# Kernel optimization log

Measured on AMD Instinct MI355X. Metric: run time of the kernel, lower is better.

## Reference

```python
import jax, jax.numpy as jnp
import numpy as np

N_HEADS = 16
D_MODEL = 1024
D_K = D_MODEL // N_HEADS
NEG_INF = -1e9


def setup_inputs() -> dict:
    key = jax.random.key(0)
    ks = jax.random.split(key, 7)
    B, S, D = 4, 2048, D_MODEL
    scale = 1.0 / np.sqrt(D)
    return {
        "query": jax.random.normal(ks[0], (B, S, D), dtype=jnp.float32),
        "key": jax.random.normal(ks[1], (B, S, D), dtype=jnp.float32),
        "value": jax.random.normal(ks[2], (B, S, D), dtype=jnp.float32),
        "Wq": jax.random.normal(ks[3], (D, D), dtype=jnp.float32) * scale,
        "Wk": jax.random.normal(ks[4], (D, D), dtype=jnp.float32) * scale,
        "Wv": jax.random.normal(ks[5], (D, D), dtype=jnp.float32) * scale,
        "Wo": jax.random.normal(ks[6], (D, D), dtype=jnp.float32) * scale,
    }


def _split_heads(x):
    # (B, S, D) -> (B, H, S, d_k)
    B, S, _ = x.shape
    return x.reshape(B, S, N_HEADS, D_K).transpose(0, 2, 1, 3)


def reference(query, key, value, Wq, Wk, Wv, Wo):
    B, S, D = query.shape
    # nn.Linear(d, d, bias=False): y = x @ W.T ; here W is stored as [out, in]
    Q = _split_heads(query @ Wq.T)
    K = _split_heads(key @ Wk.T)
    V = _split_heads(value @ Wv.T)
    scores = jnp.einsum("bhqd,bhkd->bhqk", Q, K) / jnp.sqrt(jnp.float32(D_K))
    # causal mask: 0 on/below diagonal, -1e9 above
    causal = jnp.where(
        jnp.tril(jnp.ones((S, S), dtype=bool)), 0.0, NEG_INF
    ).astype(scores.dtype)
    scores = scores + causal[None, None, :, :]
    attn = jax.nn.softmax(scores, axis=-1)
    heads = jnp.einsum("bhqk,bhkd->bhqd", attn, V)
    concat = heads.transpose(0, 2, 1, 3).reshape(B, S, D)
    out = concat @ Wo.T
    return out  # dropout p=0.0 -> identity
```

## Files before the change

### kernel.cpp

```cpp
#include <hip/hip_runtime.h>
#include <hip/hip_bf16.h>

typedef short short8 __attribute__((ext_vector_type(8)));
typedef short short4v __attribute__((ext_vector_type(4)));
typedef float floatx4 __attribute__((ext_vector_type(4)));

constexpr int BATCH = 4;
constexpr int SEQ = 2048;
constexpr int DMODEL = 1024;
constexpr int NHEADS = 16;
constexpr int DKH = 64;
constexpr int MROWS = BATCH * SEQ;
constexpr size_t NE = (size_t)MROWS * DMODEL;
constexpr size_t WE = (size_t)DMODEL * DMODEL;
constexpr float SC = 0.18033688011112042f;

__device__ __forceinline__ short f2bf(float f) {
    unsigned u = __float_as_uint(f);
    u += 0x7fffu + ((u >> 16) & 1u);
    return (short)(u >> 16);
}

__device__ __forceinline__ short2 pk2(float a, float b) {
    __hip_bfloat162 h = __float22bfloat162_rn(float2{a, b});
    short2 r;
    __builtin_memcpy(&r, &h, 4);
    return r;
}

__device__ __forceinline__ void ld16(const void* g, void* l) {
    __builtin_amdgcn_global_load_lds(
        (const __attribute__((address_space(1))) unsigned int*)g,
        (__attribute__((address_space(3))) unsigned int*)l, 16, 0, 0);
}

__device__ __forceinline__ void sync_vm4() {
    asm volatile("s_waitcnt vmcnt(4)" ::: "memory");
    __builtin_amdgcn_sched_barrier(0);
    __builtin_amdgcn_s_barrier();
    __builtin_amdgcn_sched_barrier(0);
}
__device__ __forceinline__ void sync_vm0() {
    asm volatile("s_waitcnt vmcnt(0)" ::: "memory");
    __builtin_amdgcn_sched_barrier(0);
    __builtin_amdgcn_s_barrier();
    __builtin_amdgcn_sched_barrier(0);
}

__global__ __launch_bounds__(256) void f32_to_bf16(const float* __restrict__ s,
                                                   short* __restrict__ d, int n4) {
    int i = blockIdx.x * blockDim.x + threadIdx.x;
    const int stride = gridDim.x * blockDim.x;
    for (; i < n4; i += stride) {
        float4 f = ((const float4*)s)[i];
        short4v v;
        v[0] = f2bf(f.x); v[1] = f2bf(f.y); v[2] = f2bf(f.z); v[3] = f2bf(f.w);
        ((short4v*)d)[i] = v;
    }
}

__global__ __launch_bounds__(256) void cvt2(const float* __restrict__ s0,
                                            const float* __restrict__ s1,
                                            short* __restrict__ d0,
                                            short* __restrict__ d1, int n4) {
    const float* s = blockIdx.y ? s1 : s0;
    short* d = blockIdx.y ? d1 : d0;
    int i = blockIdx.x * blockDim.x + threadIdx.x;
    const int stride = gridDim.x * blockDim.x;
    for (; i < n4; i += stride) {
        float4 f = ((const float4*)s)[i];
        short4v v;
        v[0] = f2bf(f.x); v[1] = f2bf(f.y); v[2] = f2bf(f.z); v[3] = f2bf(f.w);
        ((short4v*)d)[i] = v;
    }
}

__global__ __launch_bounds__(256) void wcvt3(const float* __restrict__ a,
                                             const float* __restrict__ b,
                                             const float* __restrict__ c,
                                             short* __restrict__ dst, int n4) {
    const float* s = (blockIdx.y == 0) ? a : (blockIdx.y == 1) ? b : c;
    const float m = (blockIdx.y == 0) ? SC : 1.0f;
    short* d = dst + (size_t)blockIdx.y * (size_t)n4 * 4;
    int i = blockIdx.x * blockDim.x + threadIdx.x;
    const int stride = gridDim.x * blockDim.x;
    for (; i < n4; i += stride) {
        float4 f = ((const float4*)s)[i];
        short4v v;
        v[0] = f2bf(f.x * m); v[1] = f2bf(f.y * m);
        v[2] = f2bf(f.z * m); v[3] = f2bf(f.w * m);
        ((short4v*)d)[i] = v;
    }
}

template <int MH, int KS, bool RB>
__device__ __forceinline__ void do_phase(const short* Ab, const short* Bb,
                                         floatx4 (&acc)[8][4], short8 (&bfr)[4],
                                         int wmw, int wnw, int lane16, int quad,
                                         int fsw) {
    if (RB) {
#pragma unroll
        for (int ni = 0; ni < 4; ++ni) {
            const int row = wnw + ni * 16 + lane16;
            bfr[ni] = *(const short8*)&Bb[KS * (256 * 32) + row * 32 +
                                          ((quad ^ fsw) * 8)];
        }
    }
    short8 af[4];
#pragma unroll
    for (int i = 0; i < 4; ++i) {
        const int row = wmw + MH * 64 + i * 16 + lane16;
        af[i] = *(const short8*)&Ab[KS * (256 * 32) + row * 32 +
                                    ((quad ^ fsw) * 8)];
    }
    __builtin_amdgcn_s_setprio(1);
#pragma unroll
    for (int i = 0; i < 4; ++i)
#pragma unroll
        for (int ni = 0; ni < 4; ++ni)
            acc[MH * 4 + i][ni] = __builtin_amdgcn_mfma_f32_16x16x32_bf16(
                af[i], bfr[ni], acc[MH * 4 + i][ni], 0, 0, 0);
    __builtin_amdgcn_s_setprio(0);
}

template <int OUT_MODE>
__device__ __forceinline__ void gemm_body(const short* A, const short* B,
                                          void* Yp) {
    __shared__ __align__(16) short Asw[2][2][256 * 32];
    __shared__ __align__(16) short Bsw[2][2][256 * 32];

    const int tid = threadIdx.x;
    const int w = tid >> 6, l = tid & 63;
    const int lane16 = l & 15, quad = l >> 4;
    const int wmw = (w >> 2) * 128, wnw = (w & 3) * 64;
    const int m0 = blockIdx.x * 256, n0 = blockIdx.y * 256;
    const int fsw = (lane16 >> 1) & 3;

    const int rr = tid >> 2;
    const int cc = (tid & 3) ^ ((rr >> 1) & 3);
    const int ldsA0 = (w * 64) * 8, ldsA1 = (512 + w * 64) * 8;

    auto stA = [&](int k0, int bufi, int ks) {
        const short* g = A + (size_t)m0 * DMODEL + k0 + ks * 32 + cc * 8;
        ld16(g + (size_t)rr * DMODEL, &Asw[bufi][ks][ldsA0]);
        ld16(g + (size_t)(rr + 128) * DMODEL, &Asw[bufi][ks][ldsA1]);
    };
    auto stB = [&](int k0, int bufi, int ks) {
        const short* g = B + (size_t)n0 * DMODEL + k0 + ks * 32 + cc * 8;
        ld16(g + (size_t)rr * DMODEL, &Bsw[bufi][ks][ldsA0]);
        ld16(g + (size_t)(rr + 128) * DMODEL, &Bsw[bufi][ks][ldsA1]);
    };

    floatx4 acc[8][4];
#pragma unroll
    for (int i = 0; i < 8; ++i)
#pragma unroll
        for (int j = 0; j < 4; ++j) acc[i][j] = {0.f, 0.f, 0.f, 0.f};

    constexpr int NT = DMODEL / 64;
    stA(0, 0, 0); stB(0, 0, 0); stA(0, 0, 1); stB(0, 0, 1);
    sync_vm4();

    short8 bfr[4];
    for (int t = 0; t < NT; ++t) {
        const int cur = t & 1, nxt = cur ^ 1;
        const short* Ab = &Asw[cur][0][0];
        const short* Bb = &Bsw[cur][0][0];
        const int k1 = (t + 1) * 64;
        const bool more = (t + 1 < NT);

        if (more) stA(k1, nxt, 0);
        do_phase<0, 0, true>(Ab, Bb, acc, bfr, wmw, wnw, lane16, quad, fsw);
        if (more) stB(k1, nxt, 0);
        do_phase<1, 0, false>(Ab, Bb, acc, bfr, wmw, wnw, lane16, quad, fsw);
        if (more) sync_vm4(); else sync_vm0();
        if (more) stA(k1, nxt, 1);
        do_phase<0, 1, true>(Ab, Bb, acc, bfr, wmw, wnw, lane16, quad, fsw);
        if (more) stB(k1, nxt, 1);
        do_phase<1, 1, false>(Ab, Bb, acc, bfr, wmw, wnw, lane16, quad, fsw);
        if (more) sync_vm4();
    }

    const int gmb = m0 + wmw, gnb = n0 + wnw;
    if (OUT_MODE == 0) {
        short* Y = (short*)Yp;
#pragma unroll
        for (int mi = 0; mi < 8; ++mi)
#pragma unroll
            for (int ni = 0; ni < 4; ++ni) {
                const int gm = gmb + mi * 16 + quad * 4;
                const int gn = gnb + ni * 16 + lane16;
#pragma unroll
                for (int r = 0; r < 4; ++r)
                    Y[(size_t)(gm + r) * DMODEL + gn] = f2bf(acc[mi][ni][r]);
            }
    } else if (OUT_MODE == 1) {
        short* Y = (short*)Yp;
#pragma unroll
        for (int mi = 0; mi < 8; ++mi)
#pragma unroll
            for (int ni = 0; ni < 4; ++ni) {
                const int gm = gmb + mi * 16 + quad * 4;
                const int gn = gnb + ni * 16 + lane16;
                const int bb = gm >> 11, ss = gm & (SEQ - 1);
                const int hh = gn >> 6, dd = gn & 63;
                const size_t base = ((size_t)(bb * NHEADS + hh) * DKH + dd) * SEQ + ss;
                short4v vv;
#pragma unroll
                for (int r = 0; r < 4; ++r) vv[r] = f2bf(acc[mi][ni][r]);
                *(short4v*)(Y + base) = vv;
            }
    } else {
        float* Y = (float*)Yp;
#pragma unroll
        for (int mi = 0; mi < 8; ++mi)
#pragma unroll
            for (int ni = 0; ni < 4; ++ni) {
                const int gm = gmb + mi * 16 + quad * 4;
                const int gn = gnb + ni * 16 + lane16;
#pragma unroll
                for (int r = 0; r < 4; ++r)
                    Y[(size_t)(gm + r) * DMODEL + gn] = acc[mi][ni][r];
            }
    }
}

template <int OUT_MODE>
__global__ __launch_bounds__(512, 2) void gemm_nt(const short* __restrict__ A,
                                                  const short* __restrict__ B,
                                                  void* __restrict__ Yp) {
    gemm_body<OUT_MODE>(A, B, Yp);
}

__global__ __launch_bounds__(512, 2) void gemm_qk(const short* __restrict__ Aq,
                                                  const short* __restrict__ Ak,
                                                  const short* __restrict__ Wqk,
                                                  short* __restrict__ Yq,
                                                  short* __restrict__ Yk) {
    const int z = blockIdx.z;
    gemm_body<0>(z ? Ak : Aq, Wqk + (size_t)z * WE, z ? Yk : Yq);
}

__global__ __launch_bounds__(256, 4) void attn_fwd(const short* __restrict__ Qb,
                                                   const short* __restrict__ Kb,
                                                   const short* __restrict__ Vt,
                                                   short* __restrict__ Oc) {
    __shared__ __align__(16) short Kl[2][64 * 64];
    __shared__ __align__(16) short Vl[2][64 * 64];
    __shared__ __align__(16) short Plds[4][16][64];

    const int bh = blockIdx.x;
    const int qt = (int)(gridDim.y - 1) - blockIdx.y;
    const int b = bh >> 4, h = bh & 15;
    const int tid = threadIdx.x;
    const int w = tid >> 6, l = tid & 63;
    const int lane16 = l & 15, quad = l >> 4;

    const short* Qrow =
        Qb + ((size_t)b * SEQ + qt * 64 + w * 16 + lane16) * DMODEL + h * DKH;
    const short8 qf0 = *(const short8*)(Qrow + quad * 8);
    const short8 qf1 = *(const short8*)(Qrow + 32 + quad * 8);

    const int r0 = tid >> 3, c0 = tid & 7;
    const int sc0 = c0 ^ (r0 & 7);
    const short* Kg = Kb + (size_t)b * SEQ * DMODEL + h * DKH;
    const short* Vg = Vt + (size_t)bh * DKH * SEQ;

    short8 kra, krb, vra, vrb;
    kra = *(const short8*)(Kg + (size_t)r0 * DMODEL + c0 * 8);
    krb = *(const short8*)(Kg + (size_t)(r0 + 32) * DMODEL + c0 * 8);
    vra = *(const short8*)(Vg + (size_t)r0 * SEQ + c0 * 8);
    vrb = *(const short8*)(Vg + (size_t)(r0 + 32) * SEQ + c0 * 8);
    *(short8*)&Kl[0][r0 * 64 + sc0 * 8] = kra;
    *(short8*)&Kl[0][(r0 + 32) * 64 + sc0 * 8] = krb;
    *(short8*)&Vl[0][r0 * 64 + sc0 * 8] = vra;
    *(short8*)&Vl[0][(r0 + 32) * 64 + sc0 * 8] = vrb;
    if (qt > 0) {
        kra = *(const short8*)(Kg + (size_t)(64 + r0) * DMODEL + c0 * 8);
        krb = *(const short8*)(Kg + (size_t)(64 + r0 + 32) * DMODEL + c0 * 8);
        vra = *(const short8*)(Vg + (size_t)r0 * SEQ + 64 + c0 * 8);
        vrb = *(const short8*)(Vg + (size_t)(r0 + 32) * SEQ + 64 + c0 * 8);
    }

    floatx4 oacc[4];
#pragma unroll
    for (int ni = 0; ni < 4; ++ni) oacc[ni] = {0.f, 0.f, 0.f, 0.f};
    float Lp = 0.f;
    const int swz = lane16 & 7;
    const int psw = lane16 & 7;

    for (int kt = 0; kt <= qt; ++kt) {
        const int cur = kt & 1;
        __syncthreads();
        if (kt < qt) {
            const int nb = cur ^ 1;
            *(short8*)&Kl[nb][r0 * 64 + sc0 * 8] = kra;
            *(short8*)&Kl[nb][(r0 + 32) * 64 + sc0 * 8] = krb;
            *(short8*)&Vl[nb][r0 * 64 + sc0 * 8] = vra;
            *(short8*)&Vl[nb][(r0 + 32) * 64 + sc0 * 8] = vrb;
            if (kt + 1 < qt) {
                const int kn = (kt + 2) * 64;
                kra = *(const short8*)(Kg + (size_t)(kn + r0) * DMODEL + c0 * 8);
                krb = *(const short8*)(Kg + (size_t)(kn + r0 + 32) * DMODEL + c0 * 8);
                vra = *(const short8*)(Vg + (size_t)r0 * SEQ + kn + c0 * 8);
                vrb = *(const short8*)(Vg + (size_t)(r0 + 32) * SEQ + kn + c0 * 8);
            }
        }

        float p[4][4];
#pragma unroll
        for (int nt = 0; nt < 4; ++nt) {
            const short* kr = &Kl[cur][(nt * 16 + lane16) * 64];
            floatx4 st = {0.f, 0.f, 0.f, 0.f};
            st = __builtin_amdgcn_mfma_f32_16x16x32_bf16(
                *(const short8*)(kr + (quad ^ swz) * 8), qf0, st, 0, 0, 0);
            st = __builtin_amdgcn_mfma_f32_16x16x32_bf16(
                *(const short8*)(kr + ((4 + quad) ^ swz) * 8), qf1, st, 0, 0, 0);
#pragma unroll
            for (int r = 0; r < 4; ++r) p[nt][r] = st[r];
        }

#pragma unroll
        for (int nt = 0; nt < 4; ++nt)
#pragma unroll
            for (int r = 0; r < 4; ++r) p[nt][r] = __builtin_amdgcn_exp2f(p[nt][r]);

        if (kt == qt) {
            const int qloc = w * 16 + lane16;
#pragma unroll
            for (int nt = 0; nt < 4; ++nt)
#pragma unroll
                for (int r = 0; r < 4; ++r)
                    if (nt * 16 + quad * 4 + r > qloc) p[nt][r] = 0.f;
        }

        float rs01 = 0.f, rs23 = 0.f;
#pragma unroll
        for (int nt = 0; nt < 4; ++nt)
#pragma unroll
            for (int r = 0; r < 4; ++r) {
                if (nt < 2) rs01 += p[nt][r]; else rs23 += p[nt][r];
            }
        Lp += rs01 + rs23;

#pragma unroll
        for (int nt = 0; nt < 4; ++nt) {
            const short2 lo = pk2(p[nt][0], p[nt][1]);
            const short2 hi = pk2(p[nt][2], p[nt][3]);
            short4v pk;
            pk[0] = lo.x; pk[1] = lo.y; pk[2] = hi.x; pk[3] = hi.y;
            const int pch = (nt * 2 + (quad >> 1)) ^ psw;
            *(short4v*)&Plds[w][lane16][pch * 8 + (quad & 1) * 4] = pk;
        }
        const short8 pf0 = *(const short8*)&Plds[w][lane16][(quad ^ psw) * 8];
        const short8 pf1 = *(const short8*)&Plds[w][lane16][((4 + quad) ^ psw) * 8];

#pragma unroll
        for (int ni = 0; ni < 4; ++ni) {
            const short* vr = &Vl[cur][(ni * 16 + lane16) * 64];
            oacc[ni] = __builtin_amdgcn_mfma_f32_16x16x32_bf16(
                pf0, *(const short8*)(vr + (quad ^ swz) * 8), oacc[ni], 0, 0, 0);
            oacc[ni] = __builtin_amdgcn_mfma_f32_16x16x32_bf16(
                pf1, *(const short8*)(vr + ((4 + quad) ^ swz) * 8), oacc[ni], 0, 0, 0);
        }
    }

    float L = Lp + __shfl_xor(Lp, 16);
    L += __shfl_xor(L, 32);
    float linv[4];
#pragma unroll
    for (int r = 0; r < 4; ++r) linv[r] = 1.f / __shfl(L, quad * 4 + r);
#pragma unroll
    for (int r = 0; r < 4; ++r) {
        const int qg = qt * 64 + w * 16 + quad * 4 + r;
#pragma unroll
        for (int ni = 0; ni < 4; ++ni)
            Oc[((size_t)b * SEQ + qg) * DMODEL + h * DKH + ni * 16 + lane16] =
                f2bf(oacc[ni][r] * linv[r]);
    }
}

extern "C" void kernel_launch(void* const* d_in, const int* in_sizes, int n_in,
                              void* d_out, int out_size, void* d_ws, size_t ws_size,
                              hipStream_t stream) {
    const float* q = (const float*)d_in[0];
    const float* k = (const float*)d_in[1];
    const float* v = (const float*)d_in[2];
    const float* Wq = (const float*)d_in[3];
    const float* Wk = (const float*)d_in[4];
    const float* Wv = (const float*)d_in[5];
    const float* Wo = (const float*)d_in[6];

    short* Qb = (short*)d_ws;
    short* Kb = Qb + NE;
    short* Vt = Kb + NE;
    short* Cc = Vt + NE;
    short* Wqb = (short*)d_out;
    short* Wkb = Wqb + WE;
    short* Wvb = Wqb + 2 * WE;
    short* Kbf = Wqb + 3 * WE;
    short* Wob = Vt;

    dim3 gg(MROWS / 256, DMODEL / 256);
    dim3 gqk(MROWS / 256, DMODEL / 256, 2);
    dim3 ga(BATCH * NHEADS, SEQ / 64);
    const int actN4 = (int)(NE / 4), wN4 = (int)(WE / 4);

    wcvt3<<<dim3(256, 3), 256, 0, stream>>>(Wq, Wk, Wv, (short*)d_out, wN4);
    cvt2<<<dim3(1024, 2), 256, 0, stream>>>(q, k, Cc, Kbf, actN4);
    gemm_qk<<<gqk, 512, 0, stream>>>(Cc, Kbf, Wqb, Qb, Kb);
    f32_to_bf16<<<2048, 256, 0, stream>>>(v, Cc, actN4);
    gemm_nt<1><<<gg, 512, 0, stream>>>(Cc, Wvb, Vt);
    attn_fwd<<<ga, 256, 0, stream>>>(Qb, Kb, Vt, Cc);
    f32_to_bf16<<<512, 256, 0, stream>>>(Wo, Wob, wN4);
    gemm_nt<2><<<gg, 512, 0, stream>>>(Cc, Wob, d_out);
}
```

Measured before the change: 328.5 us.

## Halve GEMM N-tile to 128 so the grid covers more CUs

```diff
diff --git a/kernel.cpp b/kernel.cpp
--- a/kernel.cpp
+++ b/kernel.cpp
@@ -34,8 +34,8 @@
         (__attribute__((address_space(3))) unsigned int*)l, 16, 0, 0);
 }
 
-__device__ __forceinline__ void sync_vm4() {
-    asm volatile("s_waitcnt vmcnt(4)" ::: "memory");
+__device__ __forceinline__ void sync_vm3() {
+    asm volatile("s_waitcnt vmcnt(3)" ::: "memory");
     __builtin_amdgcn_sched_barrier(0);
     __builtin_amdgcn_s_barrier();
     __builtin_amdgcn_sched_barrier(0);
@@ -93,33 +93,26 @@
     }
 }
 
-template <int MH, int KS, bool RB>
+template <int KS>
 __device__ __forceinline__ void do_phase(const short* Ab, const short* Bb,
-                                         floatx4 (&acc)[8][4], short8 (&bfr)[4],
-                                         int wmw, int wnw, int lane16, int quad,
-                                         int fsw) {
-    if (RB) {
-#pragma unroll
-        for (int ni = 0; ni < 4; ++ni) {
-            const int row = wnw + ni * 16 + lane16;
-            bfr[ni] = *(const short8*)&Bb[KS * (256 * 32) + row * 32 +
-                                          ((quad ^ fsw) * 8)];
-        }
-    }
-    short8 af[4];
-#pragma unroll
-    for (int i = 0; i < 4; ++i) {
-        const int row = wmw + MH * 64 + i * 16 + lane16;
-        af[i] = *(const short8*)&Ab[KS * (256 * 32) + row * 32 +
+                                         floatx4 (&acc)[4][4], int wm, int wn,
+                                         int lane16, int quad, int fsw) {
+    short8 af[4], bf[4];
+#pragma unroll
+    for (int i = 0; i < 4; ++i)
+        af[i] = *(const short8*)&Ab[KS * (256 * 32) + (wm + i * 16 + lane16) * 32 +
                                     ((quad ^ fsw) * 8)];
-    }
+#pragma unroll
+    for (int j = 0; j < 4; ++j)
+        bf[j] = *(const short8*)&Bb[KS * (128 * 32) + (wn + j * 16 + lane16) * 32 +
+                                    ((quad ^ fsw) * 8)];
     __builtin_amdgcn_s_setprio(1);
 #pragma unroll
     for (int i = 0; i < 4; ++i)
 #pragma unroll
-        for (int ni = 0; ni < 4; ++ni)
-            acc[MH * 4 + i][ni] = __builtin_amdgcn_mfma_f32_16x16x32_bf16(
-                af[i], bfr[ni], acc[MH * 4 + i][ni], 0, 0, 0);
+        for (int j = 0; j < 4; ++j)
+            acc[i][j] = __builtin_amdgcn_mfma_f32_16x16x32_bf16(af[i], bf[j],
+                                                                acc[i][j], 0, 0, 0);
     __builtin_amdgcn_s_setprio(0);
 }
 
@@ -127,41 +120,41 @@
 __device__ __forceinline__ void gemm_body(const short* A, const short* B,
                                           void* Yp) {
     __shared__ __align__(16) short Asw[2][2][256 * 32];
-    __shared__ __align__(16) short Bsw[2][2][256 * 32];
+    __shared__ __align__(16) short Bsw[2][2][128 * 32];
 
     const int tid = threadIdx.x;
     const int w = tid >> 6, l = tid & 63;
     const int lane16 = l & 15, quad = l >> 4;
-    const int wmw = (w >> 2) * 128, wnw = (w & 3) * 64;
-    const int m0 = blockIdx.x * 256, n0 = blockIdx.y * 256;
+    const int wm = (w >> 1) * 64, wn = (w & 1) * 64;
+    const int m0 = blockIdx.x * 256, n0 = blockIdx.y * 128;
     const int fsw = (lane16 >> 1) & 3;
 
     const int rr = tid >> 2;
     const int cc = (tid & 3) ^ ((rr >> 1) & 3);
-    const int ldsA0 = (w * 64) * 8, ldsA1 = (512 + w * 64) * 8;
+    const int ldsW0 = (w * 16) * 32;
+    const int ldsW1 = (128 + w * 16) * 32;
 
     auto stA = [&](int k0, int bufi, int ks) {
-        const short* g = A + (size_t)m0 * DMODEL + k0 + ks * 32 + cc * 8;
-        ld16(g + (size_t)rr * DMODEL, &Asw[bufi][ks][ldsA0]);
-        ld16(g + (size_t)(rr + 128) * DMODEL, &Asw[bufi][ks][ldsA1]);
+        const short* g = A + (size_t)(m0 + rr) * DMODEL + k0 + ks * 32 + cc * 8;
+        ld16(g, &Asw[bufi][ks][ldsW0]);
+        ld16(g + (size_t)128 * DMODEL, &Asw[bufi][ks][ldsW1]);
     };
     auto stB = [&](int k0, int bufi, int ks) {
-        const short* g = B + (size_t)n0 * DMODEL + k0 + ks * 32 + cc * 8;
-        ld16(g + (size_t)rr * DMODEL, &Bsw[bufi][ks][ldsA0]);
-        ld16(g + (size_t)(rr + 128) * DMODEL, &Bsw[bufi][ks][ldsA1]);
+        const short* g = B + (size_t)(n0 + rr) * DMODEL + k0 + ks * 32 + cc * 8;
+        ld16(g, &Bsw[bufi][ks][ldsW0]);
     };
 
-    floatx4 acc[8][4];
-#pragma unroll
-    for (int i = 0; i < 8; ++i)
+    floatx4 acc[4][4];
+#pragma unroll
+    for (int i = 0; i < 4; ++i)
 #pragma unroll
         for (int j = 0; j < 4; ++j) acc[i][j] = {0.f, 0.f, 0.f, 0.f};
 
     constexpr int NT = DMODEL / 64;
-    stA(0, 0, 0); stB(0, 0, 0); stA(0, 0, 1); stB(0, 0, 1);
-    sync_vm4();
-
-    short8 bfr[4];
+    stA(0, 0, 0); stB(0, 0, 0);
+    stA(0, 0, 1); stB(0, 0, 1);
+    sync_vm3();
+
     for (int t = 0; t < NT; ++t) {
         const int cur = t & 1, nxt = cur ^ 1;
         const short* Ab = &Asw[cur][0][0];
@@ -169,23 +162,19 @@
         const int k1 = (t + 1) * 64;
         const bool more = (t + 1 < NT);
 
-        if (more) stA(k1, nxt, 0);
-        do_phase<0, 0, true>(Ab, Bb, acc, bfr, wmw, wnw, lane16, quad, fsw);
-        if (more) stB(k1, nxt, 0);
-        do_phase<1, 0, false>(Ab, Bb, acc, bfr, wmw, wnw, lane16, quad, fsw);
-        if (more) sync_vm4(); else sync_vm0();
-        if (more) stA(k1, nxt, 1);
-        do_phase<0, 1, true>(Ab, Bb, acc, bfr, wmw, wnw, lane16, quad, fsw);
-        if (more) stB(k1, nxt, 1);
-        do_phase<1, 1, false>(Ab, Bb, acc, bfr, wmw, wnw, lane16, quad, fsw);
-        if (more) sync_vm4();
-    }
-
-    const int gmb = m0 + wmw, gnb = n0 + wnw;
+        if (more) { stA(k1, nxt, 0); stB(k1, nxt, 0); }
+        do_phase<0>(Ab, Bb, acc, wm, wn, lane16, quad, fsw);
+        if (more) sync_vm3(); else sync_vm0();
+        if (more) { stA(k1, nxt, 1); stB(k1, nxt, 1); }
+        do_phase<1>(Ab, Bb, acc, wm, wn, lane16, quad, fsw);
+        if (more) sync_vm3();
+    }
+
+    const int gmb = m0 + wm, gnb = n0 + wn;
     if (OUT_MODE == 0) {
         short* Y = (short*)Yp;
 #pragma unroll
-        for (int mi = 0; mi < 8; ++mi)
+        for (int mi = 0; mi < 4; ++mi)
 #pragma unroll
             for (int ni = 0; ni < 4; ++ni) {
                 const int gm = gmb + mi * 16 + quad * 4;
@@ -197,7 +186,7 @@
     } else if (OUT_MODE == 1) {
         short* Y = (short*)Yp;
 #pragma unroll
-        for (int mi = 0; mi < 8; ++mi)
+        for (int mi = 0; mi < 4; ++mi)
 #pragma unroll
             for (int ni = 0; ni < 4; ++ni) {
                 const int gm = gmb + mi * 16 + quad * 4;
@@ -213,7 +202,7 @@
     } else {
         float* Y = (float*)Yp;
 #pragma unroll
-        for (int mi = 0; mi < 8; ++mi)
+        for (int mi = 0; mi < 4; ++mi)
 #pragma unroll
             for (int ni = 0; ni < 4; ++ni) {
                 const int gm = gmb + mi * 16 + quad * 4;
@@ -401,8 +390,8 @@
     short* Kbf = Wqb + 3 * WE;
     short* Wob = Vt;
 
-    dim3 gg(MROWS / 256, DMODEL / 256);
-    dim3 gqk(MROWS / 256, DMODEL / 256, 2);
+    dim3 gg(MROWS / 256, DMODEL / 128);
+    dim3 gqk(MROWS / 256, DMODEL / 128, 2);
     dim3 ga(BATCH * NHEADS, SEQ / 64);
     const int actN4 = (int)(NE / 4), wN4 = (int)(WE / 4);
 
```

After: 329.0 us. No clear change (+0.2%).
